# Optimization experiments

Hardware: AMD Instinct MI355X
Metric: run time of the kernel (lower is better)

## Reference

```python
import jax, jax.numpy as jnp
import numpy as np

N_HEADS = 16
HEAD_DIM = 64
EMB = 1024
B, S = 2, 2048


def setup_inputs() -> dict:
    key = jax.random.key(0)
    ks = jax.random.split(key, 8)
    inner = N_HEADS * HEAD_DIM
    return {
        "query": jax.random.normal(ks[0], (B, S, EMB), dtype=jnp.float32),
        "key": jax.random.normal(ks[1], (B, S, EMB), dtype=jnp.float32),
        "value": jax.random.normal(ks[2], (B, S, EMB), dtype=jnp.float32),
        "positional_mask": jnp.ones((B, S), dtype=bool),
        "future_mask": 1,
        # torch nn.Linear weight layout: (out_features, in_features)
        "Wq": jax.random.normal(ks[3], (inner, EMB), dtype=jnp.float32) * 0.02,
        "Wk": jax.random.normal(ks[4], (inner, EMB), dtype=jnp.float32) * 0.02,
        "Wv": jax.random.normal(ks[5], (inner, EMB), dtype=jnp.float32) * 0.02,
        "Wo": jax.random.normal(ks[6], (EMB, inner), dtype=jnp.float32) * 0.02,
        "bo": jax.random.normal(ks[7], (EMB,), dtype=jnp.float32) * 0.02,
    }


def reference(query, key, value, positional_mask, future_mask, Wq, Wk, Wv, Wo, bo):
    batch, seq = query.shape[:2]
    # project and split heads: (B, S, H, D)
    q = (query @ Wq.T).reshape(batch, seq, N_HEADS, HEAD_DIM)
    k = (key @ Wk.T).reshape(batch, seq, N_HEADS, HEAD_DIM)
    v = (value @ Wv.T).reshape(batch, seq, N_HEADS, HEAD_DIM)
    scale = 1.0 / np.sqrt(HEAD_DIM).astype(np.float32)
    # (B, H, Sq, Sk)
    weights = jnp.einsum("bqhd,bkhd->bhqk", q, k) * scale
    neg_inf = jnp.float32(-jnp.inf)
    # additive key-position mask
    reweight = jnp.where(positional_mask, jnp.float32(0.0), neg_inf)  # (B, S)
    weights = weights + reweight[:, None, None, :]
    if future_mask:
        causal = jnp.triu(jnp.full((seq, seq), neg_inf, dtype=weights.dtype), k=1)
        weights = weights + causal
    weights = jax.nn.softmax(weights, axis=-1)
    out = jnp.einsum("bhqk,bkhd->bqhd", weights, v).reshape(batch, seq, -1)
    return out @ Wo.T + bo
```

## Files before the change

### kernel.cpp

```cpp
#include <hip/hip_runtime.h>
#include <hip/hip_bf16.h>
#include <math.h>

#define EMB    1024
#define NH     16
#define HD     64
#define BATCH  2
#define SEQ    2048
#define MTOK   (BATCH * SEQ)

typedef __bf16 bf16_t;
typedef __bf16 bf16x8 __attribute__((ext_vector_type(8)));
typedef __bf16 bf16x4 __attribute__((ext_vector_type(4)));
typedef float  f32x4  __attribute__((ext_vector_type(4)));

#define NEG_BIG (-1.0e30f)

#define GLD16(g, l) __builtin_amdgcn_global_load_lds(                     \
    (const __attribute__((address_space(1))) void*)(g),                   \
    (__attribute__((address_space(3))) void*)(l), 16, 0, 0)

__device__ inline bf16x8 ld_frag64(const bf16_t* __restrict__ p) {
    const bf16x4 lo = *(const bf16x4*)p;
    const bf16x4 hi = *(const bf16x4*)(p + 4);
    bf16x8 r;
#pragma unroll
    for (int j = 0; j < 4; ++j) { r[j] = lo[j]; r[j + 4] = hi[j]; }
    return r;
}

__global__ __launch_bounds__(256) void cast_bf16(
    const float* __restrict__ q, const float* __restrict__ k,
    const float* __restrict__ v, const float* __restrict__ wq,
    const float* __restrict__ wk, const float* __restrict__ wv,
    const float* __restrict__ wo, bf16_t* __restrict__ ws)
{
    const size_t g = ((size_t)blockIdx.x * 256 + threadIdx.x) * 8;
    const size_t BIG = (size_t)1 << 22;
    const size_t SML = (size_t)1 << 20;
    const float* src;
    bf16_t* dst;
    size_t off;
    if (g < 3 * BIG) {
        const int s = (int)(g >> 22);
        src = s == 0 ? q : (s == 1 ? k : v);
        dst = ws + (size_t)s * BIG;
        off = g & (BIG - 1);
    } else {
        const size_t h = g - 3 * BIG;
        const int s = (int)(h >> 20);
        src = s == 0 ? wq : (s == 1 ? wk : (s == 2 ? wv : wo));
        dst = ws + 3 * BIG + (size_t)s * SML;
        off = h & (SML - 1);
    }
    const f32x4 f0 = *(const f32x4*)(src + off);
    const f32x4 f1 = *(const f32x4*)(src + off + 4);
    bf16x8 r;
#pragma unroll
    for (int j = 0; j < 4; ++j) { r[j] = (bf16_t)f0[j]; r[j + 4] = (bf16_t)f1[j]; }
    *(bf16x8*)(dst + off) = r;
}

template<int BM, int BN, bool OUTF32>
__global__ __launch_bounds__(256) void gemm_dma(
    const bf16_t* __restrict__ A, const bf16_t* __restrict__ Wb,
    const float* __restrict__ bias, void* __restrict__ Cp,
    size_t sA, size_t sW, size_t sC)
{
    constexpr int K = EMB, N = EMB;
    constexpr int MT = BM / 32, NT = BN / 32;
    constexpr int IA = BM / 64, IB = BN / 64;
    __shared__ __align__(16) bf16_t As[2][BM * 32];
    __shared__ __align__(16) bf16_t Bs[2][BN * 32];

    const int tid  = threadIdx.x;
    const int wave = tid >> 6;
    const int lane = tid & 63;
    const int l15  = lane & 15;
    const int quad = lane >> 4;
    const int z    = blockIdx.z;
    A  += (size_t)z * sA;
    Wb += (size_t)z * sW;

    const int m0 = blockIdx.y * BM;
    const int n0 = blockIdx.x * BN;
    const int wm = (wave >> 1) * (BM / 2);
    const int wn = (wave & 1) * (BN / 2);

    const int lrow = lane >> 2;
    const int scol = ((lane & 3) ^ (lrow & 3)) * 8;
    const bf16_t* gA = A  + (size_t)(m0 + wave * (BM / 4) + lrow) * K + scol;
    const bf16_t* gB = Wb + (size_t)(n0 + wave * (BN / 4) + lrow) * K + scol;
    const int loffA = wave * (BM / 4) * 32;
    const int loffB = wave * (BN / 4) * 32;

    f32x4 acc[MT][NT] = {};
    const int xq = (quad ^ (l15 & 3)) * 8;

#pragma unroll
    for (int i = 0; i < IA; ++i) GLD16(gA + (size_t)i * 16 * K, &As[0][loffA + i * 512]);
#pragma unroll
    for (int i = 0; i < IB; ++i) GLD16(gB + (size_t)i * 16 * K, &Bs[0][loffB + i * 512]);

    for (int t = 0; t < K / 32; ++t) {
        __syncthreads();
        if (t + 1 < K / 32) {
            const size_t ko = (size_t)(t + 1) * 32;
            const int nb = (t + 1) & 1;
#pragma unroll
            for (int i = 0; i < IA; ++i)
                GLD16(gA + ko + (size_t)i * 16 * K, &As[nb][loffA + i * 512]);
#pragma unroll
            for (int i = 0; i < IB; ++i)
                GLD16(gB + ko + (size_t)i * 16 * K, &Bs[nb][loffB + i * 512]);
        }
        const int buf = t & 1;
        bf16x8 af[MT], bfr[NT];
#pragma unroll
        for (int mt = 0; mt < MT; ++mt)
            af[mt] = *(const bf16x8*)&As[buf][(wm + mt * 16 + l15) * 32 + xq];
#pragma unroll
        for (int nt = 0; nt < NT; ++nt)
            bfr[nt] = *(const bf16x8*)&Bs[buf][(wn + nt * 16 + l15) * 32 + xq];
#pragma unroll
        for (int mt = 0; mt < MT; ++mt)
#pragma unroll
            for (int nt = 0; nt < NT; ++nt)
                acc[mt][nt] = __builtin_amdgcn_mfma_f32_16x16x32_bf16(
                    af[mt], bfr[nt], acc[mt][nt], 0, 0, 0);
    }

    const size_t cb = (size_t)z * sC;
#pragma unroll
    for (int nt = 0; nt < NT; ++nt) {
        const int col = n0 + wn + nt * 16 + l15;
        const float bv = bias ? bias[col] : 0.0f;
#pragma unroll
        for (int mt = 0; mt < MT; ++mt) {
#pragma unroll
            for (int r = 0; r < 4; ++r) {
                const int row = m0 + wm + mt * 16 + quad * 4 + r;
                const float v = acc[mt][nt][r] + bv;
                if constexpr (OUTF32) ((float*) Cp)[cb + (size_t)row * N + col] = v;
                else                  ((bf16_t*)Cp)[cb + (size_t)row * N + col] = (bf16_t)v;
            }
        }
    }
}

__global__ __launch_bounds__(256) void attn_flash(
    const bf16_t* __restrict__ Q, const bf16_t* __restrict__ Km,
    const bf16_t* __restrict__ V, bf16_t* __restrict__ O)
{
    __shared__ __align__(16) bf16_t Ks[64 * 64];
    __shared__ __align__(16) bf16_t Vs[64][76];
    __shared__ bf16_t Pb[4][16 * 68];
    __shared__ bf16_t Ob[4][16 * 72];

    const int tid  = threadIdx.x;
    const int wave = tid >> 6;
    const int lane = tid & 63;
    const int l15  = lane & 15;
    const int quad = lane >> 4;
    const int b = blockIdx.z, h = blockIdx.y;

    const bf16_t* Qb = Q  + ((size_t)b * SEQ) * EMB + h * HD;
    const bf16_t* Kb = Km + ((size_t)b * SEQ) * EMB + h * HD;
    const bf16_t* Vb = V  + ((size_t)b * SEQ) * EMB + h * HD;

    const int krow = lane >> 3;
    const int kcol = ((lane & 7) ^ krow) * 8;
    const int vk   = wave * 16;
    bf16_t* P = Pb[wave];
    const float scale = 0.125f;
    const int sw = l15 & 7;

    for (int ph = 0; ph < 2; ++ph) {
        const int qi = (ph == 0) ? (int)blockIdx.x : 31 - (int)blockIdx.x;
        const int qbase = qi * 64 + wave * 16;
        const int qg = qbase + l15;
        const int nkt = qi + 1;

        const bf16x8 qlo = *(const bf16x8*)(Qb + (size_t)(qbase + l15) * EMB + quad * 8);
        const bf16x8 qhi = *(const bf16x8*)(Qb + (size_t)(qbase + l15) * EMB + 32 + quad * 8);

        float m_s = NEG_BIG, l_s = 0.0f;
        f32x4 o[4] = {};

        for (int kt = 0; kt < nkt; ++kt) {
            const int kb = kt * 64;

#pragma unroll
            for (int i = 0; i < 2; ++i) {
                const int r0 = wave * 16 + i * 8;
                GLD16(Kb + (size_t)(kb + r0 + krow) * EMB + kcol, &Ks[r0 * 64]);
            }
#pragma unroll
            for (int t = 0; t < 4; ++t) {
                bf16x4 vv;
#pragma unroll
                for (int j = 0; j < 4; ++j)
                    vv[j] = Vb[(size_t)(kb + vk + t * 4 + j) * EMB + lane];
                *(bf16x4*)&Vs[lane][vk + t * 4] = vv;
            }
            __syncthreads();

            f32x4 s[4];
            __builtin_amdgcn_s_setprio(1);
#pragma unroll
            for (int t2 = 0; t2 < 4; ++t2) {
                const int row = t2 * 16 + l15;
                const bf16x8 klo = *(const bf16x8*)&Ks[row * 64 + ((quad ^ sw) * 8)];
                const bf16x8 khi = *(const bf16x8*)&Ks[row * 64 + (((4 + quad) ^ sw) * 8)];
                f32x4 a = {};
                a = __builtin_amdgcn_mfma_f32_16x16x32_bf16(klo, qlo, a, 0, 0, 0);
                a = __builtin_amdgcn_mfma_f32_16x16x32_bf16(khi, qhi, a, 0, 0, 0);
                s[t2] = a;
            }
            __builtin_amdgcn_s_setprio(0);

            float sc[16];
#pragma unroll
            for (int t2 = 0; t2 < 4; ++t2)
#pragma unroll
                for (int r = 0; r < 4; ++r)
                    sc[t2 * 4 + r] = s[t2][r] * scale;
            if (kt == nkt - 1) {
#pragma unroll
                for (int t2 = 0; t2 < 4; ++t2)
#pragma unroll
                    for (int r = 0; r < 4; ++r)
                        if (kb + t2 * 16 + quad * 4 + r > qg)
                            sc[t2 * 4 + r] = NEG_BIG;
            }
            float mx = sc[0];
#pragma unroll
            for (int j = 1; j < 16; ++j) mx = fmaxf(mx, sc[j]);
            mx = fmaxf(mx, __shfl_xor(mx, 16, 64));
            mx = fmaxf(mx, __shfl_xor(mx, 32, 64));
            if (!__all(mx - m_s <= 8.0f)) {
                const float mnew  = fmaxf(m_s, mx);
                const float alpha = __expf(m_s - mnew);
                l_s *= alpha;
#pragma unroll
                for (int dt = 0; dt < 4; ++dt)
#pragma unroll
                    for (int r = 0; r < 4; ++r) o[dt][r] *= alpha;
                m_s = mnew;
            }
            float e[16], rs = 0.0f;
#pragma unroll
            for (int j = 0; j < 16; ++j) { e[j] = __expf(sc[j] - m_s); rs += e[j]; }
            rs += __shfl_xor(rs, 16, 64);
            rs += __shfl_xor(rs, 32, 64);
            l_s += rs;

#pragma unroll
            for (int t2 = 0; t2 < 4; ++t2) {
                bf16x4 p4;
#pragma unroll
                for (int r = 0; r < 4; ++r) p4[r] = (bf16_t)e[t2 * 4 + r];
                *(bf16x4*)&P[l15 * 68 + t2 * 16 + quad * 4] = p4;
            }
            __asm__ volatile("s_waitcnt lgkmcnt(0)" ::: "memory");
            const bf16x8 pb0 = ld_frag64(&P[l15 * 68 + quad * 8]);
            const bf16x8 pb1 = ld_frag64(&P[l15 * 68 + 32 + quad * 8]);

            __builtin_amdgcn_s_setprio(1);
#pragma unroll
            for (int dt = 0; dt < 4; ++dt) {
                const bf16x8 va0 = ld_frag64(&Vs[dt * 16 + l15][quad * 8]);
                const bf16x8 va1 = ld_frag64(&Vs[dt * 16 + l15][32 + quad * 8]);
                o[dt] = __builtin_amdgcn_mfma_f32_16x16x32_bf16(va0, pb0, o[dt], 0, 0, 0);
                o[dt] = __builtin_amdgcn_mfma_f32_16x16x32_bf16(va1, pb1, o[dt], 0, 0, 0);
            }
            __builtin_amdgcn_s_setprio(0);
            __syncthreads();
        }

        const float inv = 1.0f / l_s;
        bf16_t* OT = Ob[wave];
#pragma unroll
        for (int dt = 0; dt < 4; ++dt) {
            bf16x4 pk;
#pragma unroll
            for (int r = 0; r < 4; ++r) pk[r] = (bf16_t)(o[dt][r] * inv);
            *(bf16x4*)&OT[l15 * 72 + dt * 16 + quad * 4] = pk;
        }
        __asm__ volatile("s_waitcnt lgkmcnt(0)" ::: "memory");
        const bf16x8 r0 = *(const bf16x8*)&OT[l15 * 72 + quad * 16];
        const bf16x8 r1 = *(const bf16x8*)&OT[l15 * 72 + quad * 16 + 8];
        bf16_t* dst = O + ((size_t)b * SEQ + qbase + l15) * EMB + h * HD + quad * 16;
        *(bf16x8*)dst       = r0;
        *(bf16x8*)(dst + 8) = r1;
    }
}

extern "C" void kernel_launch(void* const* d_in, const int* in_sizes, int n_in,
                              void* d_out, int out_size, void* d_ws, size_t ws_size,
                              hipStream_t stream)
{
    const float* query = (const float*)d_in[0];
    const float* key   = (const float*)d_in[1];
    const float* value = (const float*)d_in[2];
    const float* Wq = (const float*)d_in[5];
    const float* Wk = (const float*)d_in[6];
    const float* Wv = (const float*)d_in[7];
    const float* Wo = (const float*)d_in[8];
    const float* bo = (const float*)d_in[9];

    const size_t BIG = (size_t)1 << 22, SML = (size_t)1 << 20;
    bf16_t* ws  = (bf16_t*)d_ws;
    bf16_t* qc  = ws;
    bf16_t* kc  = qc + BIG;
    bf16_t* vc  = kc + BIG;
    bf16_t* wqc = vc + BIG;
    bf16_t* wkc = wqc + SML;
    bf16_t* wvc = wkc + SML;
    bf16_t* woc = wvc + SML;
    bf16_t* Qp  = woc + SML;
    bf16_t* Kp  = Qp + BIG;
    bf16_t* Vp  = Kp + BIG;
    bf16_t* Ab  = Vp + BIG;

    const dim3 blk(256);

    cast_bf16<<<dim3(8192), blk, 0, stream>>>(query, key, value, Wq, Wk, Wv, Wo, ws);

    gemm_dma<128, 128, false><<<dim3(EMB / 128, MTOK / 128, 3), blk, 0, stream>>>(
        qc, wqc, nullptr, Qp, BIG, SML, BIG);

    attn_flash<<<dim3(SEQ / 128, NH, BATCH), blk, 0, stream>>>(Qp, Kp, Vp, Ab);

    gemm_dma<64, 128, true><<<dim3(EMB / 128, MTOK / 64, 1), blk, 0, stream>>>(
        Ab, woc, bo, (float*)d_out, 0, 0, 0);
}
```

Before: 241.4 us.

## Triple-buffer GEMM loads and double-buffer K/V in flash attention

The projection GEMM moves from double to triple-buffered LDS staging, prefetching two tiles ahead. It waits with explicit vmcnt counts and a raw barrier instead of a full __syncthreads, and raises wave priority around the MFMAs. The attention kernel double-buffers K and V so the next tile's global loads overlap the current tile's QK and PV math, dropping one barrier per iteration. Softmax switches to exp2 with a log2e-folded scale, a tree max reduction and a wider rescale threshold. This costs more LDS per block, which may reduce occupancy.

```diff
diff --git a/kernel.cpp b/kernel.cpp
--- a/kernel.cpp
+++ b/kernel.cpp
@@ -70,8 +70,9 @@
     constexpr int K = EMB, N = EMB;
     constexpr int MT = BM / 32, NT = BN / 32;
     constexpr int IA = BM / 64, IB = BN / 64;
-    __shared__ __align__(16) bf16_t As[2][BM * 32];
-    __shared__ __align__(16) bf16_t Bs[2][BN * 32];
+    constexpr int nT = K / 32;
+    __shared__ __align__(16) bf16_t As[3][BM * 32];
+    __shared__ __align__(16) bf16_t Bs[3][BN * 32];
 
     const int tid  = threadIdx.x;
     const int wave = tid >> 6;
@@ -97,37 +98,49 @@
     f32x4 acc[MT][NT] = {};
     const int xq = (quad ^ (l15 & 3)) * 8;
 
-#pragma unroll
-    for (int i = 0; i < IA; ++i) GLD16(gA + (size_t)i * 16 * K, &As[0][loffA + i * 512]);
-#pragma unroll
-    for (int i = 0; i < IB; ++i) GLD16(gB + (size_t)i * 16 * K, &Bs[0][loffB + i * 512]);
-
-    for (int t = 0; t < K / 32; ++t) {
-        __syncthreads();
-        if (t + 1 < K / 32) {
-            const size_t ko = (size_t)(t + 1) * 32;
-            const int nb = (t + 1) & 1;
-#pragma unroll
-            for (int i = 0; i < IA; ++i)
-                GLD16(gA + ko + (size_t)i * 16 * K, &As[nb][loffA + i * 512]);
-#pragma unroll
-            for (int i = 0; i < IB; ++i)
-                GLD16(gB + ko + (size_t)i * 16 * K, &Bs[nb][loffB + i * 512]);
-        }
-        const int buf = t & 1;
+    auto stage = [&](int t, int b3) {
+        const size_t ko = (size_t)t * 32;
+#pragma unroll
+        for (int i = 0; i < IA; ++i)
+            GLD16(gA + ko + (size_t)i * 16 * K, &As[b3][loffA + i * 512]);
+#pragma unroll
+        for (int i = 0; i < IB; ++i)
+            GLD16(gB + ko + (size_t)i * 16 * K, &Bs[b3][loffB + i * 512]);
+    };
+
+    stage(0, 0);
+    stage(1, 1);
+
+    int cur = 0;
+    for (int t = 0; t < nT; ++t) {
+        if (t == nT - 1) {
+            asm volatile("s_waitcnt vmcnt(0)" ::: "memory");
+        } else {
+            asm volatile("s_waitcnt vmcnt(%0)" :: "n"(IA + IB) : "memory");
+        }
+        __builtin_amdgcn_s_barrier();
+
         bf16x8 af[MT], bfr[NT];
 #pragma unroll
         for (int mt = 0; mt < MT; ++mt)
-            af[mt] = *(const bf16x8*)&As[buf][(wm + mt * 16 + l15) * 32 + xq];
+            af[mt] = *(const bf16x8*)&As[cur][(wm + mt * 16 + l15) * 32 + xq];
 #pragma unroll
         for (int nt = 0; nt < NT; ++nt)
-            bfr[nt] = *(const bf16x8*)&Bs[buf][(wn + nt * 16 + l15) * 32 + xq];
+            bfr[nt] = *(const bf16x8*)&Bs[cur][(wn + nt * 16 + l15) * 32 + xq];
+        __builtin_amdgcn_s_setprio(1);
 #pragma unroll
         for (int mt = 0; mt < MT; ++mt)
 #pragma unroll
             for (int nt = 0; nt < NT; ++nt)
                 acc[mt][nt] = __builtin_amdgcn_mfma_f32_16x16x32_bf16(
                     af[mt], bfr[nt], acc[mt][nt], 0, 0, 0);
+        __builtin_amdgcn_s_setprio(0);
+
+        if (t + 2 < nT) {
+            int b3 = cur + 2; if (b3 >= 3) b3 -= 3;
+            stage(t + 2, b3);
+        }
+        if (++cur == 3) cur = 0;
     }
 
     const size_t cb = (size_t)z * sC;
@@ -152,8 +165,8 @@
     const bf16_t* __restrict__ Q, const bf16_t* __restrict__ Km,
     const bf16_t* __restrict__ V, bf16_t* __restrict__ O)
 {
-    __shared__ __align__(16) bf16_t Ks[64 * 64];
-    __shared__ __align__(16) bf16_t Vs[64][76];
+    __shared__ __align__(16) bf16_t Ks[2][64 * 64];
+    __shared__ __align__(16) bf16_t Vs[2][64][76];
     __shared__ bf16_t Pb[4][16 * 68];
     __shared__ bf16_t Ob[4][16 * 72];
 
@@ -172,7 +185,7 @@
     const int kcol = ((lane & 7) ^ krow) * 8;
     const int vk   = wave * 16;
     bf16_t* P = Pb[wave];
-    const float scale = 0.125f;
+    const float scale2 = 0.18033688011112042f;
     const int sw = l15 & 7;
 
     for (int ph = 0; ph < 2; ++ph) {
@@ -187,31 +200,52 @@
         float m_s = NEG_BIG, l_s = 0.0f;
         f32x4 o[4] = {};
 
+        __syncthreads();
+#pragma unroll
+        for (int i = 0; i < 2; ++i) {
+            const int r0 = wave * 16 + i * 8;
+            GLD16(Kb + (size_t)(r0 + krow) * EMB + kcol, &Ks[0][r0 * 64]);
+        }
+        {
+            bf16x4 vr[4];
+#pragma unroll
+            for (int t = 0; t < 4; ++t)
+#pragma unroll
+                for (int j = 0; j < 4; ++j)
+                    vr[t][j] = Vb[(size_t)(vk + t * 4 + j) * EMB + lane];
+#pragma unroll
+            for (int t = 0; t < 4; ++t)
+                *(bf16x4*)&Vs[0][lane][vk + t * 4] = vr[t];
+        }
+
         for (int kt = 0; kt < nkt; ++kt) {
+            const int cur = kt & 1, nb = cur ^ 1;
             const int kb = kt * 64;
-
-#pragma unroll
-            for (int i = 0; i < 2; ++i) {
-                const int r0 = wave * 16 + i * 8;
-                GLD16(Kb + (size_t)(kb + r0 + krow) * EMB + kcol, &Ks[r0 * 64]);
-            }
-#pragma unroll
-            for (int t = 0; t < 4; ++t) {
-                bf16x4 vv;
-#pragma unroll
-                for (int j = 0; j < 4; ++j)
-                    vv[j] = Vb[(size_t)(kb + vk + t * 4 + j) * EMB + lane];
-                *(bf16x4*)&Vs[lane][vk + t * 4] = vv;
-            }
             __syncthreads();
+
+            bf16x4 vr[4];
+            const bool more = (kt + 1) < nkt;
+            if (more) {
+                const int kb1 = kb + 64;
+#pragma unroll
+                for (int i = 0; i < 2; ++i) {
+                    const int r0 = wave * 16 + i * 8;
+                    GLD16(Kb + (size_t)(kb1 + r0 + krow) * EMB + kcol, &Ks[nb][r0 * 64]);
+                }
+#pragma unroll
+                for (int t = 0; t < 4; ++t)
+#pragma unroll
+                    for (int j = 0; j < 4; ++j)
+                        vr[t][j] = Vb[(size_t)(kb1 + vk + t * 4 + j) * EMB + lane];
+            }
 
             f32x4 s[4];
             __builtin_amdgcn_s_setprio(1);
 #pragma unroll
             for (int t2 = 0; t2 < 4; ++t2) {
                 const int row = t2 * 16 + l15;
-                const bf16x8 klo = *(const bf16x8*)&Ks[row * 64 + ((quad ^ sw) * 8)];
-                const bf16x8 khi = *(const bf16x8*)&Ks[row * 64 + (((4 + quad) ^ sw) * 8)];
+                const bf16x8 klo = *(const bf16x8*)&Ks[cur][row * 64 + ((quad ^ sw) * 8)];
+                const bf16x8 khi = *(const bf16x8*)&Ks[cur][row * 64 + (((4 + quad) ^ sw) * 8)];
                 f32x4 a = {};
                 a = __builtin_amdgcn_mfma_f32_16x16x32_bf16(klo, qlo, a, 0, 0, 0);
                 a = __builtin_amdgcn_mfma_f32_16x16x32_bf16(khi, qhi, a, 0, 0, 0);
@@ -219,12 +253,18 @@
             }
             __builtin_amdgcn_s_setprio(0);
 
+            if (more) {
+#pragma unroll
+                for (int t = 0; t < 4; ++t)
+                    *(bf16x4*)&Vs[nb][lane][vk + t * 4] = vr[t];
+            }
+
             float sc[16];
 #pragma unroll
             for (int t2 = 0; t2 < 4; ++t2)
 #pragma unroll
                 for (int r = 0; r < 4; ++r)
-                    sc[t2 * 4 + r] = s[t2][r] * scale;
+                    sc[t2 * 4 + r] = s[t2][r] * scale2;
             if (kt == nkt - 1) {
 #pragma unroll
                 for (int t2 = 0; t2 < 4; ++t2)
@@ -233,14 +273,16 @@
                         if (kb + t2 * 16 + quad * 4 + r > qg)
                             sc[t2 * 4 + r] = NEG_BIG;
             }
-            float mx = sc[0];
-#pragma unroll
-            for (int j = 1; j < 16; ++j) mx = fmaxf(mx, sc[j]);
+            float m0a = fmaxf(fmaxf(sc[0],  sc[1]),  fmaxf(sc[2],  sc[3]));
+            float m1a = fmaxf(fmaxf(sc[4],  sc[5]),  fmaxf(sc[6],  sc[7]));
+            float m2a = fmaxf(fmaxf(sc[8],  sc[9]),  fmaxf(sc[10], sc[11]));
+            float m3a = fmaxf(fmaxf(sc[12], sc[13]), fmaxf(sc[14], sc[15]));
+            float mx = fmaxf(fmaxf(m0a, m1a), fmaxf(m2a, m3a));
             mx = fmaxf(mx, __shfl_xor(mx, 16, 64));
             mx = fmaxf(mx, __shfl_xor(mx, 32, 64));
-            if (!__all(mx - m_s <= 8.0f)) {
+            if (!__all(mx - m_s <= 11.5f)) {
                 const float mnew  = fmaxf(m_s, mx);
-                const float alpha = __expf(m_s - mnew);
+                const float alpha = __builtin_amdgcn_exp2f(m_s - mnew);
                 l_s *= alpha;
 #pragma unroll
                 for (int dt = 0; dt < 4; ++dt)
@@ -250,7 +292,10 @@
             }
             float e[16], rs = 0.0f;
 #pragma unroll
-            for (int j = 0; j < 16; ++j) { e[j] = __expf(sc[j] - m_s); rs += e[j]; }
+            for (int j = 0; j < 16; ++j) {
+                e[j] = __builtin_amdgcn_exp2f(sc[j] - m_s);
+                rs += e[j];
+            }
             rs += __shfl_xor(rs, 16, 64);
             rs += __shfl_xor(rs, 32, 64);
             l_s += rs;
@@ -269,13 +314,12 @@
             __builtin_amdgcn_s_setprio(1);
 #pragma unroll
             for (int dt = 0; dt < 4; ++dt) {
-                const bf16x8 va0 = ld_frag64(&Vs[dt * 16 + l15][quad * 8]);
-                const bf16x8 va1 = ld_frag64(&Vs[dt * 16 + l15][32 + quad * 8]);
+                const bf16x8 va0 = ld_frag64(&Vs[cur][dt * 16 + l15][quad * 8]);
+                const bf16x8 va1 = ld_frag64(&Vs[cur][dt * 16 + l15][32 + quad * 8]);
                 o[dt] = __builtin_amdgcn_mfma_f32_16x16x32_bf16(va0, pb0, o[dt], 0, 0, 0);
                 o[dt] = __builtin_amdgcn_mfma_f32_16x16x32_bf16(va1, pb1, o[dt], 0, 0, 0);
             }
             __builtin_amdgcn_s_setprio(0);
-            __syncthreads();
         }
 
         const float inv = 1.0f / l_s;
```

After: 239.7 us. No clear change (-0.7%).
